# Optimization experiments

Hardware: AMD Instinct MI355X
Metric: run time of the kernel (lower is better)

The kernel has to match this reference:

```python
import jax, jax.numpy as jnp
import numpy as np

NUM_EXPERTS = 8
TOP_K = 2
HIDDEN = 1024
INTER = 4096  # ffn_hidden_size; fc1 produces 2*INTER for gated swiglu
TOKENS = 128


def setup_inputs() -> dict:
    key = jax.random.key(0)
    k1, k2, k3, k4 = jax.random.split(key, 4)
    hidden_states = jax.random.normal(k1, (TOKENS, HIDDEN), dtype=jnp.float32)
    routing = jax.random.normal(k2, (TOKENS, NUM_EXPERTS), dtype=jnp.float32)
    # fc1: [E, 2*inter, hidden] (rows 0:inter = up/linear path fed to act, inter:2*inter = gate)
    w1 = jax.random.normal(k3, (NUM_EXPERTS, 2 * INTER, HIDDEN), dtype=jnp.float32) * 0.02
    # fc2: [E, hidden, inter]
    w2 = jax.random.normal(k4, (NUM_EXPERTS, HIDDEN, INTER), dtype=jnp.float32) * 0.02
    return {"hidden_states": hidden_states, "routing": routing, "w1": w1, "w2": w2}


def reference(hidden_states, routing, w1, w2):
    # Top-k routing with renormalization (TRT-LLM RENORMALIZE mode):
    # softmax over all experts, take top-k probs, rescale to sum to 1.
    probs = jax.nn.softmax(routing, axis=-1)                  # [T, E]
    topv, topi = jax.lax.top_k(probs, TOP_K)                  # [T, k]
    scales = topv / jnp.sum(topv, axis=-1, keepdims=True)     # [T, k]

    num_experts = w1.shape[0]
    inter = w2.shape[2]
    out = jnp.zeros_like(hidden_states)
    # Fixed small loop over experts (structurally distinct weights); tokens stay vectorized.
    for e in range(num_experts):
        # combined routing coefficient of expert e for every token (0 if not selected)
        coef = jnp.sum(jnp.where(topi == e, scales, 0.0), axis=-1)   # [T]
        h = jnp.einsum('th,oh->to', hidden_states, w1[e])            # [T, 2*inter]
        act = jax.nn.silu(h[:, :inter]) * h[:, inter:]               # swiglu
        y = jnp.einsum('ti,hi->th', act, w2[e])                      # [T, hidden]
        out = out + coef[:, None] * y
    return out
```

## Files before the change

kernel.cpp:

```cpp
#include <hip/hip_runtime.h>
#include <hip/hip_bf16.h>

#define T_TOK 128
#define N_EXP 8
#define HID   1024
#define INTER 4096

typedef __bf16 bf16x8 __attribute__((ext_vector_type(8)));
typedef __bf16 bf16x4 __attribute__((ext_vector_type(4)));
typedef float  f32x4  __attribute__((ext_vector_type(4)));

__global__ void route_kernel(const float* __restrict__ routing,
                             int* __restrict__ cnt,
                             int* __restrict__ tok,
                             float* __restrict__ scal) {
    int t = threadIdx.x;
    int wave = t >> 6, lane = t & 63;

    float l[N_EXP];
#pragma unroll
    for (int e = 0; e < N_EXP; ++e) l[e] = routing[t * N_EXP + e];

    int i1 = 0; float v1 = l[0];
#pragma unroll
    for (int e = 1; e < N_EXP; ++e) if (l[e] > v1) { v1 = l[e]; i1 = e; }
    int i2 = -1; float v2 = -1e30f;
#pragma unroll
    for (int e = 0; e < N_EXP; ++e) if (e != i1 && l[e] > v2) { v2 = l[e]; i2 = e; }

    float s1 = 1.0f / (1.0f + __expf(v2 - v1));
    float s2 = 1.0f - s1;

    __shared__ unsigned long long wmask[2][N_EXP];
#pragma unroll
    for (int e = 0; e < N_EXP; ++e) {
        bool sel = (i1 == e) || (i2 == e);
        unsigned long long m = __ballot(sel);
        if (lane == 0) wmask[wave][e] = m;
    }
    __syncthreads();
#pragma unroll
    for (int e = 0; e < N_EXP; ++e) {
        bool sel = (i1 == e) || (i2 == e);
        unsigned long long m = __ballot(sel);
        int pre  = __popcll(m & ((1ull << lane) - 1ull));
        int base = (wave == 1) ? __popcll(wmask[0][e]) : 0;
        if (sel) {
            int slot = base + pre;
            tok [e * T_TOK + slot] = t;
            scal[e * T_TOK + slot] = (i1 == e) ? s1 : s2;
        }
        if (t == 0) cnt[e] = __popcll(wmask[0][e]) + __popcll(wmask[1][e]);
    }
}

__global__ void prep_kernel(const float* __restrict__ hidden,
                            const int* __restrict__ cnt,
                            const int* __restrict__ tok,
                            __bf16* __restrict__ abuf) {
    int b = blockIdx.x;
    int e = b >> 7, s = b & 127;
    if (s >= cnt[e]) return;
    int t = tok[e * T_TOK + s];
    const float4* src = (const float4*)(hidden + (size_t)t * HID);
    __bf16* dst = abuf + ((size_t)e * T_TOK + s) * HID;
#pragma unroll
    for (int it = 0; it < 4; ++it) {
        int idx = it * 64 + threadIdx.x;
        float4 v = src[idx];
        bf16x4 pk;
        pk[0] = (__bf16)v.x; pk[1] = (__bf16)v.y;
        pk[2] = (__bf16)v.z; pk[3] = (__bf16)v.w;
        *(bf16x4*)(dst + idx * 4) = pk;
    }
}

__device__ __forceinline__ bf16x8 cvt8(float4 a, float4 b) {
    bf16x8 r;
    r[0] = (__bf16)a.x; r[1] = (__bf16)a.y; r[2] = (__bf16)a.z; r[3] = (__bf16)a.w;
    r[4] = (__bf16)b.x; r[5] = (__bf16)b.y; r[6] = (__bf16)b.z; r[7] = (__bf16)b.w;
    return r;
}

template<int MG>
__device__ __forceinline__ void g1_loop(const float* __restrict__ bl,
                                        const float* __restrict__ bg,
                                        const __bf16* __restrict__ ap,
                                        f32x4* accl, f32x4* accg) {
#pragma unroll 2
    for (int k0 = 0; k0 < HID; k0 += 32) {
        float4 fl0 = *(const float4*)(bl + k0);
        float4 fl1 = *(const float4*)(bl + k0 + 4);
        float4 fg0 = *(const float4*)(bg + k0);
        float4 fg1 = *(const float4*)(bg + k0 + 4);
        bf16x8 A[MG];
#pragma unroll
        for (int m = 0; m < MG; ++m)
            A[m] = *(const bf16x8*)(ap + (size_t)m * 16 * HID + k0);
        bf16x8 BL = cvt8(fl0, fl1);
        bf16x8 BG = cvt8(fg0, fg1);
#pragma unroll
        for (int m = 0; m < MG; ++m) {
            accl[m] = __builtin_amdgcn_mfma_f32_16x16x32_bf16(A[m], BL, accl[m], 0, 0, 0);
            accg[m] = __builtin_amdgcn_mfma_f32_16x16x32_bf16(A[m], BG, accg[m], 0, 0, 0);
        }
    }
}

__global__ __launch_bounds__(256) void gemm1_kernel(
    const float* __restrict__ w1,
    const int* __restrict__ cnt,
    const __bf16* __restrict__ abuf,
    __bf16* __restrict__ act) {
    int bx = blockIdx.x;
    int e  = bx >> 6, nb = bx & 63;
    int wave = threadIdx.x >> 6, lane = threadIdx.x & 63;
    int n0 = nb * 64 + wave * 16;
    int c  = cnt[e];
    if (c == 0) return;
    int mgs = (c + 15) >> 4;
    int lr = lane & 15;
    int lq = lane >> 4;

    const float* bl = w1 + ((size_t)e * 2 * INTER + n0 + lr) * HID + lq * 8;
    const float* bg = bl + (size_t)INTER * HID;
    const __bf16* ap = abuf + ((size_t)e * T_TOK + lr) * HID + lq * 8;

    f32x4 accl[8], accg[8];
#pragma unroll
    for (int m = 0; m < 8; ++m) {
        accl[m] = (f32x4){0.f, 0.f, 0.f, 0.f};
        accg[m] = (f32x4){0.f, 0.f, 0.f, 0.f};
    }

    switch (mgs) {
        case 1: g1_loop<1>(bl, bg, ap, accl, accg); break;
        case 2: g1_loop<2>(bl, bg, ap, accl, accg); break;
        case 3: g1_loop<3>(bl, bg, ap, accl, accg); break;
        case 4: g1_loop<4>(bl, bg, ap, accl, accg); break;
        case 5: g1_loop<5>(bl, bg, ap, accl, accg); break;
        case 6: g1_loop<6>(bl, bg, ap, accl, accg); break;
        case 7: g1_loop<7>(bl, bg, ap, accl, accg); break;
        default: g1_loop<8>(bl, bg, ap, accl, accg); break;
    }

#pragma unroll
    for (int m = 0; m < 8; ++m) {
        if (m * 16 < c) {
#pragma unroll
            for (int r = 0; r < 4; ++r) {
                int slot = m * 16 + lq * 4 + r;
                if (slot < c) {
                    float lin  = accl[m][r];
                    float gate = accg[m][r];
                    float a = lin * (1.0f / (1.0f + __expf(-lin))) * gate;
                    act[((size_t)e * T_TOK + slot) * INTER + n0 + lr] = (__bf16)a;
                }
            }
        }
    }
}

#define KSPLIT 4
#define KCH (INTER / KSPLIT)

template<int MG>
__device__ __forceinline__ void g2_loop(const float* __restrict__ bp,
                                        const __bf16* __restrict__ ap,
                                        f32x4* acc) {
#pragma unroll 2
    for (int k0 = 0; k0 < KCH; k0 += 32) {
        float4 f0 = *(const float4*)(bp + k0);
        float4 f1 = *(const float4*)(bp + k0 + 4);
        bf16x8 A[MG];
#pragma unroll
        for (int m = 0; m < MG; ++m)
            A[m] = *(const bf16x8*)(ap + (size_t)m * 16 * INTER + k0);
        bf16x8 B = cvt8(f0, f1);
#pragma unroll
        for (int m = 0; m < MG; ++m)
            acc[m] = __builtin_amdgcn_mfma_f32_16x16x32_bf16(A[m], B, acc[m], 0, 0, 0);
    }
}

__global__ __launch_bounds__(256) void gemm2_kernel(
    const float* __restrict__ w2,
    const int* __restrict__ cnt,
    const int* __restrict__ tok,
    const float* __restrict__ scal,
    const __bf16* __restrict__ act,
    float* __restrict__ out) {
    int bx = blockIdx.x;
    int ks = bx & (KSPLIT - 1), nb = (bx >> 2) & 15, e = bx >> 6;
    int wave = threadIdx.x >> 6, lane = threadIdx.x & 63;
    int n0 = nb * 64 + wave * 16;
    int c  = cnt[e];
    if (c == 0) return;
    int mgs = (c + 15) >> 4;
    int lr = lane & 15, lq = lane >> 4;

    const float* bp = w2 + ((size_t)e * HID + n0 + lr) * INTER + ks * KCH + lq * 8;
    const __bf16* ap = act + ((size_t)e * T_TOK + lr) * INTER + ks * KCH + lq * 8;

    f32x4 acc[8];
#pragma unroll
    for (int m = 0; m < 8; ++m) acc[m] = (f32x4){0.f, 0.f, 0.f, 0.f};

    switch (mgs) {
        case 1: g2_loop<1>(bp, ap, acc); break;
        case 2: g2_loop<2>(bp, ap, acc); break;
        case 3: g2_loop<3>(bp, ap, acc); break;
        case 4: g2_loop<4>(bp, ap, acc); break;
        case 5: g2_loop<5>(bp, ap, acc); break;
        case 6: g2_loop<6>(bp, ap, acc); break;
        case 7: g2_loop<7>(bp, ap, acc); break;
        default: g2_loop<8>(bp, ap, acc); break;
    }

#pragma unroll
    for (int m = 0; m < 8; ++m) {
        if (m * 16 < c) {
#pragma unroll
            for (int r = 0; r < 4; ++r) {
                int slot = m * 16 + lq * 4 + r;
                if (slot < c) {
                    int   t    = tok [e * T_TOK + slot];
                    float coef = scal[e * T_TOK + slot];
                    atomicAdd(&out[(size_t)t * HID + n0 + lr], coef * acc[m][r]);
                }
            }
        }
    }
}

extern "C" void kernel_launch(void* const* d_in, const int* in_sizes, int n_in,
                              void* d_out, int out_size, void* d_ws, size_t ws_size,
                              hipStream_t stream) {
    const float* hidden  = (const float*)d_in[0];
    const float* routing = (const float*)d_in[1];
    const float* w1      = (const float*)d_in[2];
    const float* w2      = (const float*)d_in[3];
    float* out = (float*)d_out;

    char* ws = (char*)d_ws;
    int*    cnt  = (int*)ws;
    int*    tok  = (int*)(ws + 64);
    float*  scal = (float*)(ws + 64 + 4096);
    __bf16* abuf = (__bf16*)(ws + 16384);
    __bf16* act  = (__bf16*)(ws + 16384 + (size_t)2 * 1024 * 1024);

    hipMemsetAsync(d_out, 0, (size_t)out_size * sizeof(float), stream);

    route_kernel<<<1, 128, 0, stream>>>(routing, cnt, tok, scal);
    prep_kernel<<<N_EXP * T_TOK, 64, 0, stream>>>(hidden, cnt, tok, abuf);
    gemm1_kernel<<<N_EXP * 64, 256, 0, stream>>>(w1, cnt, abuf, act);
    gemm2_kernel<<<N_EXP * 16 * KSPLIT, 256, 0, stream>>>(w2, cnt, tok, scal, act, out);
}
```

Baseline: 484.6 us.

## Stage fp32 weight tiles through swizzled LDS as bf16 with coalesced row loads

Both GEMM kernels stop having each lane load strided 32-byte chunks of fp32 weights straight from global memory. Each block now loads a 64-row by 256-column weight tile with fully coalesced float4 row reads, converts it to bf16, and writes it into XOR-swizzled shared memory. The MFMA fragments are then read from LDS. This is meant to improve global memory coalescing on the weight stream, which dominates traffic. In exchange it adds two barriers per K-chunk with no double buffering, so loads and compute no longer overlap, and it uses more LDS per block.

```diff
diff --git a/kernel.cpp b/kernel.cpp
--- a/kernel.cpp
+++ b/kernel.cpp
@@ -75,35 +75,60 @@
     }
 }
 
-__device__ __forceinline__ bf16x8 cvt8(float4 a, float4 b) {
-    bf16x8 r;
-    r[0] = (__bf16)a.x; r[1] = (__bf16)a.y; r[2] = (__bf16)a.z; r[3] = (__bf16)a.w;
-    r[4] = (__bf16)b.x; r[5] = (__bf16)b.y; r[6] = (__bf16)b.z; r[7] = (__bf16)b.w;
-    return r;
-}
+#define BK1 256
+#define LDS_ROWB (BK1 * 2)
 
 template<int MG>
-__device__ __forceinline__ void g1_loop(const float* __restrict__ bl,
-                                        const float* __restrict__ bg,
+__device__ __forceinline__ void g1_body(const float* __restrict__ pl,
+                                        const float* __restrict__ pg,
                                         const __bf16* __restrict__ ap,
-                                        f32x4* accl, f32x4* accg) {
-#pragma unroll 2
-    for (int k0 = 0; k0 < HID; k0 += 32) {
-        float4 fl0 = *(const float4*)(bl + k0);
-        float4 fl1 = *(const float4*)(bl + k0 + 4);
-        float4 fg0 = *(const float4*)(bg + k0);
-        float4 fg1 = *(const float4*)(bg + k0 + 4);
-        bf16x8 A[MG];
-#pragma unroll
-        for (int m = 0; m < MG; ++m)
-            A[m] = *(const bf16x8*)(ap + (size_t)m * 16 * HID + k0);
-        bf16x8 BL = cvt8(fl0, fl1);
-        bf16x8 BG = cvt8(fg0, fg1);
-#pragma unroll
-        for (int m = 0; m < MG; ++m) {
-            accl[m] = __builtin_amdgcn_mfma_f32_16x16x32_bf16(A[m], BL, accl[m], 0, 0, 0);
-            accg[m] = __builtin_amdgcn_mfma_f32_16x16x32_bf16(A[m], BG, accg[m], 0, 0, 0);
-        }
+                                        char* __restrict__ ldsb,
+                                        int wave, int lane,
+                                        f32x4* __restrict__ accl,
+                                        f32x4* __restrict__ accg) {
+    const int lr = lane & 15, lq = lane >> 4;
+    const int sread = (lr & 7) << 4;
+    const char* blp = ldsb + (size_t)(wave * 16 + lr) * LDS_ROWB;
+    const char* bgp = blp + (size_t)64 * LDS_ROWB;
+
+    for (int ks = 0; ks < HID; ks += BK1) {
+#pragma unroll 8
+        for (int it = 0; it < 16; ++it) {
+            int row = it * 4 + wave;
+            float4 v = *(const float4*)(pl + (size_t)row * HID + ks);
+            bf16x4 pk;
+            pk[0] = (__bf16)v.x; pk[1] = (__bf16)v.y;
+            pk[2] = (__bf16)v.z; pk[3] = (__bf16)v.w;
+            *(bf16x4*)(ldsb + (size_t)row * LDS_ROWB +
+                       ((lane * 8) ^ ((row & 7) << 4))) = pk;
+        }
+#pragma unroll 8
+        for (int it = 0; it < 16; ++it) {
+            int row = it * 4 + wave;
+            float4 v = *(const float4*)(pg + (size_t)row * HID + ks);
+            bf16x4 pk;
+            pk[0] = (__bf16)v.x; pk[1] = (__bf16)v.y;
+            pk[2] = (__bf16)v.z; pk[3] = (__bf16)v.w;
+            *(bf16x4*)(ldsb + (size_t)(64 + row) * LDS_ROWB +
+                       ((lane * 8) ^ ((row & 7) << 4))) = pk;
+        }
+        __syncthreads();
+#pragma unroll
+        for (int kk = 0; kk < BK1; kk += 32) {
+            int off = (kk * 2 + lq * 16) ^ sread;
+            bf16x8 BL = *(const bf16x8*)(blp + off);
+            bf16x8 BG = *(const bf16x8*)(bgp + off);
+            bf16x8 A[MG];
+#pragma unroll
+            for (int m = 0; m < MG; ++m)
+                A[m] = *(const bf16x8*)(ap + (size_t)m * 16 * HID + ks + kk);
+#pragma unroll
+            for (int m = 0; m < MG; ++m) {
+                accl[m] = __builtin_amdgcn_mfma_f32_16x16x32_bf16(A[m], BL, accl[m], 0, 0, 0);
+                accg[m] = __builtin_amdgcn_mfma_f32_16x16x32_bf16(A[m], BG, accg[m], 0, 0, 0);
+            }
+        }
+        __syncthreads();
     }
 }
 
@@ -112,18 +137,20 @@
     const int* __restrict__ cnt,
     const __bf16* __restrict__ abuf,
     __bf16* __restrict__ act) {
+    __shared__ __align__(16) __bf16 lds[128 * BK1];
     int bx = blockIdx.x;
     int e  = bx >> 6, nb = bx & 63;
     int wave = threadIdx.x >> 6, lane = threadIdx.x & 63;
-    int n0 = nb * 64 + wave * 16;
     int c  = cnt[e];
     if (c == 0) return;
     int mgs = (c + 15) >> 4;
     int lr = lane & 15;
     int lq = lane >> 4;
-
-    const float* bl = w1 + ((size_t)e * 2 * INTER + n0 + lr) * HID + lq * 8;
-    const float* bg = bl + (size_t)INTER * HID;
+    int n0b = nb * 64;
+
+    const float* w1e = w1 + (size_t)e * 2 * INTER * HID;
+    const float* pl  = w1e + (size_t)n0b * HID + lane * 4;
+    const float* pg  = w1e + ((size_t)INTER + n0b) * HID + lane * 4;
     const __bf16* ap = abuf + ((size_t)e * T_TOK + lr) * HID + lq * 8;
 
     f32x4 accl[8], accg[8];
@@ -133,17 +160,19 @@
         accg[m] = (f32x4){0.f, 0.f, 0.f, 0.f};
     }
 
+    char* ldsb = (char*)lds;
     switch (mgs) {
-        case 1: g1_loop<1>(bl, bg, ap, accl, accg); break;
-        case 2: g1_loop<2>(bl, bg, ap, accl, accg); break;
-        case 3: g1_loop<3>(bl, bg, ap, accl, accg); break;
-        case 4: g1_loop<4>(bl, bg, ap, accl, accg); break;
-        case 5: g1_loop<5>(bl, bg, ap, accl, accg); break;
-        case 6: g1_loop<6>(bl, bg, ap, accl, accg); break;
-        case 7: g1_loop<7>(bl, bg, ap, accl, accg); break;
-        default: g1_loop<8>(bl, bg, ap, accl, accg); break;
-    }
-
+        case 1: g1_body<1>(pl, pg, ap, ldsb, wave, lane, accl, accg); break;
+        case 2: g1_body<2>(pl, pg, ap, ldsb, wave, lane, accl, accg); break;
+        case 3: g1_body<3>(pl, pg, ap, ldsb, wave, lane, accl, accg); break;
+        case 4: g1_body<4>(pl, pg, ap, ldsb, wave, lane, accl, accg); break;
+        case 5: g1_body<5>(pl, pg, ap, ldsb, wave, lane, accl, accg); break;
+        case 6: g1_body<6>(pl, pg, ap, ldsb, wave, lane, accl, accg); break;
+        case 7: g1_body<7>(pl, pg, ap, ldsb, wave, lane, accl, accg); break;
+        default: g1_body<8>(pl, pg, ap, ldsb, wave, lane, accl, accg); break;
+    }
+
+    int n0 = n0b + wave * 16;
 #pragma unroll
     for (int m = 0; m < 8; ++m) {
         if (m * 16 < c) {
@@ -165,21 +194,40 @@
 #define KCH (INTER / KSPLIT)
 
 template<int MG>
-__device__ __forceinline__ void g2_loop(const float* __restrict__ bp,
+__device__ __forceinline__ void g2_body(const float* __restrict__ pw,
                                         const __bf16* __restrict__ ap,
-                                        f32x4* acc) {
-#pragma unroll 2
-    for (int k0 = 0; k0 < KCH; k0 += 32) {
-        float4 f0 = *(const float4*)(bp + k0);
-        float4 f1 = *(const float4*)(bp + k0 + 4);
-        bf16x8 A[MG];
-#pragma unroll
-        for (int m = 0; m < MG; ++m)
-            A[m] = *(const bf16x8*)(ap + (size_t)m * 16 * INTER + k0);
-        bf16x8 B = cvt8(f0, f1);
-#pragma unroll
-        for (int m = 0; m < MG; ++m)
-            acc[m] = __builtin_amdgcn_mfma_f32_16x16x32_bf16(A[m], B, acc[m], 0, 0, 0);
+                                        char* __restrict__ ldsb,
+                                        int wave, int lane,
+                                        f32x4* __restrict__ acc) {
+    const int lr = lane & 15, lq = lane >> 4;
+    const int sread = (lr & 7) << 4;
+    const char* bp = ldsb + (size_t)(wave * 16 + lr) * LDS_ROWB;
+
+    for (int ks = 0; ks < KCH; ks += BK1) {
+#pragma unroll 8
+        for (int it = 0; it < 16; ++it) {
+            int row = it * 4 + wave;
+            float4 v = *(const float4*)(pw + (size_t)row * INTER + ks);
+            bf16x4 pk;
+            pk[0] = (__bf16)v.x; pk[1] = (__bf16)v.y;
+            pk[2] = (__bf16)v.z; pk[3] = (__bf16)v.w;
+            *(bf16x4*)(ldsb + (size_t)row * LDS_ROWB +
+                       ((lane * 8) ^ ((row & 7) << 4))) = pk;
+        }
+        __syncthreads();
+#pragma unroll
+        for (int kk = 0; kk < BK1; kk += 32) {
+            int off = (kk * 2 + lq * 16) ^ sread;
+            bf16x8 B = *(const bf16x8*)(bp + off);
+            bf16x8 A[MG];
+#pragma unroll
+            for (int m = 0; m < MG; ++m)
+                A[m] = *(const bf16x8*)(ap + (size_t)m * 16 * INTER + ks + kk);
+#pragma unroll
+            for (int m = 0; m < MG; ++m)
+                acc[m] = __builtin_amdgcn_mfma_f32_16x16x32_bf16(A[m], B, acc[m], 0, 0, 0);
+        }
+        __syncthreads();
     }
 }
 
@@ -190,33 +238,36 @@
     const float* __restrict__ scal,
     const __bf16* __restrict__ act,
     float* __restrict__ out) {
+    __shared__ __align__(16) __bf16 lds[64 * BK1];
     int bx = blockIdx.x;
-    int ks = bx & (KSPLIT - 1), nb = (bx >> 2) & 15, e = bx >> 6;
+    int ksc = bx & (KSPLIT - 1), nb = (bx >> 2) & 15, e = bx >> 6;
     int wave = threadIdx.x >> 6, lane = threadIdx.x & 63;
-    int n0 = nb * 64 + wave * 16;
     int c  = cnt[e];
     if (c == 0) return;
     int mgs = (c + 15) >> 4;
     int lr = lane & 15, lq = lane >> 4;
-
-    const float* bp = w2 + ((size_t)e * HID + n0 + lr) * INTER + ks * KCH + lq * 8;
-    const __bf16* ap = act + ((size_t)e * T_TOK + lr) * INTER + ks * KCH + lq * 8;
+    int n0b = nb * 64;
+
+    const float* pw  = w2 + ((size_t)e * HID + n0b) * INTER + ksc * KCH + lane * 4;
+    const __bf16* ap = act + ((size_t)e * T_TOK + lr) * INTER + ksc * KCH + lq * 8;
 
     f32x4 acc[8];
 #pragma unroll
     for (int m = 0; m < 8; ++m) acc[m] = (f32x4){0.f, 0.f, 0.f, 0.f};
 
+    char* ldsb = (char*)lds;
     switch (mgs) {
-        case 1: g2_loop<1>(bp, ap, acc); break;
-        case 2: g2_loop<2>(bp, ap, acc); break;
-        case 3: g2_loop<3>(bp, ap, acc); break;
-        case 4: g2_loop<4>(bp, ap, acc); break;
-        case 5: g2_loop<5>(bp, ap, acc); break;
-        case 6: g2_loop<6>(bp, ap, acc); break;
-        case 7: g2_loop<7>(bp, ap, acc); break;
-        default: g2_loop<8>(bp, ap, acc); break;
-    }
-
+        case 1: g2_body<1>(pw, ap, ldsb, wave, lane, acc); break;
+        case 2: g2_body<2>(pw, ap, ldsb, wave, lane, acc); break;
+        case 3: g2_body<3>(pw, ap, ldsb, wave, lane, acc); break;
+        case 4: g2_body<4>(pw, ap, ldsb, wave, lane, acc); break;
+        case 5: g2_body<5>(pw, ap, ldsb, wave, lane, acc); break;
+        case 6: g2_body<6>(pw, ap, ldsb, wave, lane, acc); break;
+        case 7: g2_body<7>(pw, ap, ldsb, wave, lane, acc); break;
+        default: g2_body<8>(pw, ap, ldsb, wave, lane, acc); break;
+    }
+
+    int n0 = n0b + wave * 16;
 #pragma unroll
     for (int m = 0; m < 8; ++m) {
         if (m * 16 < c) {
```

Result: no change. 483.7 us (-0.2%).

## Stage fp32 weights through double-buffered LDS via async global_load_lds

Applied to the files above, without the earlier changes.

Both GEMM kernels now stream fp32 weight tiles into a double-buffered LDS ring using the direct global-to-LDS load builtin, with an XOR swizzle on the 16-byte chunk index to avoid bank conflicts. Each wave then reads its B fragments from LDS and converts them to bf16 for the MFMA instructions. The goal is to overlap weight fetches with compute and issue wider, more coalesced reads for the memory-bound weight stream. In exchange it adds per-stage block barriers and 64KB or 32KB of LDS per block, which may lower occupancy.

```diff
diff --git a/kernel.cpp b/kernel.cpp
--- a/kernel.cpp
+++ b/kernel.cpp
@@ -9,6 +9,11 @@
 typedef __bf16 bf16x8 __attribute__((ext_vector_type(8)));
 typedef __bf16 bf16x4 __attribute__((ext_vector_type(4)));
 typedef float  f32x4  __attribute__((ext_vector_type(4)));
+
+#define GLOAD_LDS16(gp, lp)                                                   \
+    __builtin_amdgcn_global_load_lds(                                         \
+        (const __attribute__((address_space(1))) void*)(gp),                  \
+        (__attribute__((address_space(3))) void*)(lp), 16, 0, 0)
 
 __global__ void route_kernel(const float* __restrict__ routing,
                              int* __restrict__ cnt,
@@ -82,28 +87,60 @@
     return r;
 }
 
+
+__device__ __forceinline__ void g1_stage(const char* pe, const char* po,
+                                         char* dstbase, int ksb) {
+#pragma unroll
+    for (int i = 0; i < 8; ++i) {
+        const char* src = ((i & 1) ? po : pe) + (size_t)(i * 4) * (HID * 4) + ksb;
+        GLOAD_LDS16(src, dstbase + i * 1024);
+    }
+}
+
 template<int MG>
-__device__ __forceinline__ void g1_loop(const float* __restrict__ bl,
-                                        const float* __restrict__ bg,
-                                        const __bf16* __restrict__ ap,
-                                        f32x4* accl, f32x4* accg) {
-#pragma unroll 2
-    for (int k0 = 0; k0 < HID; k0 += 32) {
-        float4 fl0 = *(const float4*)(bl + k0);
-        float4 fl1 = *(const float4*)(bl + k0 + 4);
-        float4 fg0 = *(const float4*)(bg + k0);
-        float4 fg1 = *(const float4*)(bg + k0 + 4);
+__device__ __forceinline__ void g1_compute(const char* __restrict__ buf,
+                                           const __bf16* __restrict__ ap,
+                                           int ksf, int wave, int lr,
+                                           const int* __restrict__ coff,
+                                           f32x4* __restrict__ accl,
+                                           f32x4* __restrict__ accg) {
+    const char* rowL = buf + (size_t)(wave * 16 + lr) * 256;
+    const char* rowG = rowL + 64 * 256;
+#pragma unroll
+    for (int kk = 0; kk < 2; ++kk) {
+        float4 l0 = *(const float4*)(rowL + coff[kk * 2]);
+        float4 l1 = *(const float4*)(rowL + coff[kk * 2 + 1]);
+        float4 g0 = *(const float4*)(rowG + coff[kk * 2]);
+        float4 g1 = *(const float4*)(rowG + coff[kk * 2 + 1]);
+        bf16x8 BL = cvt8(l0, l1);
+        bf16x8 BG = cvt8(g0, g1);
         bf16x8 A[MG];
 #pragma unroll
         for (int m = 0; m < MG; ++m)
-            A[m] = *(const bf16x8*)(ap + (size_t)m * 16 * HID + k0);
-        bf16x8 BL = cvt8(fl0, fl1);
-        bf16x8 BG = cvt8(fg0, fg1);
+            A[m] = *(const bf16x8*)(ap + (size_t)m * 16 * HID + ksf + kk * 32);
 #pragma unroll
         for (int m = 0; m < MG; ++m) {
             accl[m] = __builtin_amdgcn_mfma_f32_16x16x32_bf16(A[m], BL, accl[m], 0, 0, 0);
             accg[m] = __builtin_amdgcn_mfma_f32_16x16x32_bf16(A[m], BG, accg[m], 0, 0, 0);
         }
+    }
+}
+
+template<int MG>
+__device__ __forceinline__ void g1_pipe(const char* pe, const char* po,
+                                        char* ldsbase, int ldrow_off,
+                                        const __bf16* ap, const int* coff,
+                                        int wave, int lr,
+                                        f32x4* accl, f32x4* accg) {
+    g1_stage(pe, po, ldsbase + ldrow_off, 0);
+    __syncthreads();
+#pragma unroll 2
+    for (int s = 0; s < 16; ++s) {
+        int b = s & 1;
+        if (s + 1 < 16)
+            g1_stage(pe, po, ldsbase + (b ^ 1) * 32768 + ldrow_off, (s + 1) * 256);
+        g1_compute<MG>(ldsbase + b * 32768, ap, s * 64, wave, lr, coff, accl, accg);
+        __syncthreads();
     }
 }
 
@@ -112,18 +149,33 @@
     const int* __restrict__ cnt,
     const __bf16* __restrict__ abuf,
     __bf16* __restrict__ act) {
+    __shared__ __align__(16) char lds[2 * 32768];
     int bx = blockIdx.x;
     int e  = bx >> 6, nb = bx & 63;
     int wave = threadIdx.x >> 6, lane = threadIdx.x & 63;
-    int n0 = nb * 64 + wave * 16;
     int c  = cnt[e];
     if (c == 0) return;
     int mgs = (c + 15) >> 4;
     int lr = lane & 15;
     int lq = lane >> 4;
-
-    const float* bl = w1 + ((size_t)e * 2 * INTER + n0 + lr) * HID + lq * 8;
-    const float* bg = bl + (size_t)INTER * HID;
+    int n0b = nb * 64;
+
+    int lhi = lane >> 4;
+    int lch = lane & 15;
+    int half = wave & 1, gate = wave >> 1;
+    const char* w1b  = (const char*)w1 + (size_t)e * 2 * INTER * HID * 4;
+    const char* srcb = w1b + ((size_t)gate * INTER + n0b + half * 32 + lhi) * (size_t)(HID * 4);
+    const char* pe = srcb + ((lch ^ lhi) << 4);
+    const char* po = srcb + ((lch ^ (4 + lhi)) << 4);
+    int ldrow_off = (half * 32 + gate * 64) * 256;
+
+    int coff[4];
+#pragma unroll
+    for (int kk = 0; kk < 2; ++kk)
+#pragma unroll
+        for (int j = 0; j < 2; ++j)
+            coff[kk * 2 + j] = ((kk * 8 + lq * 2 + j) ^ (lr & 7)) << 4;
+
     const __bf16* ap = abuf + ((size_t)e * T_TOK + lr) * HID + lq * 8;
 
     f32x4 accl[8], accg[8];
@@ -134,16 +186,17 @@
     }
 
     switch (mgs) {
-        case 1: g1_loop<1>(bl, bg, ap, accl, accg); break;
-        case 2: g1_loop<2>(bl, bg, ap, accl, accg); break;
-        case 3: g1_loop<3>(bl, bg, ap, accl, accg); break;
-        case 4: g1_loop<4>(bl, bg, ap, accl, accg); break;
-        case 5: g1_loop<5>(bl, bg, ap, accl, accg); break;
-        case 6: g1_loop<6>(bl, bg, ap, accl, accg); break;
-        case 7: g1_loop<7>(bl, bg, ap, accl, accg); break;
-        default: g1_loop<8>(bl, bg, ap, accl, accg); break;
-    }
-
+        case 1: g1_pipe<1>(pe, po, lds, ldrow_off, ap, coff, wave, lr, accl, accg); break;
+        case 2: g1_pipe<2>(pe, po, lds, ldrow_off, ap, coff, wave, lr, accl, accg); break;
+        case 3: g1_pipe<3>(pe, po, lds, ldrow_off, ap, coff, wave, lr, accl, accg); break;
+        case 4: g1_pipe<4>(pe, po, lds, ldrow_off, ap, coff, wave, lr, accl, accg); break;
+        case 5: g1_pipe<5>(pe, po, lds, ldrow_off, ap, coff, wave, lr, accl, accg); break;
+        case 6: g1_pipe<6>(pe, po, lds, ldrow_off, ap, coff, wave, lr, accl, accg); break;
+        case 7: g1_pipe<7>(pe, po, lds, ldrow_off, ap, coff, wave, lr, accl, accg); break;
+        default: g1_pipe<8>(pe, po, lds, ldrow_off, ap, coff, wave, lr, accl, accg); break;
+    }
+
+    int n0 = n0b + wave * 16;
 #pragma unroll
     for (int m = 0; m < 8; ++m) {
         if (m * 16 < c) {
@@ -152,8 +205,8 @@
                 int slot = m * 16 + lq * 4 + r;
                 if (slot < c) {
                     float lin  = accl[m][r];
-                    float gate = accg[m][r];
-                    float a = lin * (1.0f / (1.0f + __expf(-lin))) * gate;
+                    float gate_v = accg[m][r];
+                    float a = lin * (1.0f / (1.0f + __expf(-lin))) * gate_v;
                     act[((size_t)e * T_TOK + slot) * INTER + n0 + lr] = (__bf16)a;
                 }
             }
@@ -164,22 +217,52 @@
 #define KSPLIT 4
 #define KCH (INTER / KSPLIT)
 
+__device__ __forceinline__ void g2_stage(const char* pe, const char* po,
+                                         char* dstbase, int ksb) {
+#pragma unroll
+    for (int i = 0; i < 4; ++i) {
+        const char* src = ((i & 1) ? po : pe) + (size_t)(i * 4) * (INTER * 4) + ksb;
+        GLOAD_LDS16(src, dstbase + i * 1024);
+    }
+}
+
 template<int MG>
-__device__ __forceinline__ void g2_loop(const float* __restrict__ bp,
-                                        const __bf16* __restrict__ ap,
-                                        f32x4* acc) {
-#pragma unroll 2
-    for (int k0 = 0; k0 < KCH; k0 += 32) {
-        float4 f0 = *(const float4*)(bp + k0);
-        float4 f1 = *(const float4*)(bp + k0 + 4);
+__device__ __forceinline__ void g2_compute(const char* __restrict__ buf,
+                                           const __bf16* __restrict__ ap,
+                                           int ksf, int wave, int lr,
+                                           const int* __restrict__ coff,
+                                           f32x4* __restrict__ acc) {
+    const char* row = buf + (size_t)(wave * 16 + lr) * 256;
+#pragma unroll
+    for (int kk = 0; kk < 2; ++kk) {
+        float4 q0 = *(const float4*)(row + coff[kk * 2]);
+        float4 q1 = *(const float4*)(row + coff[kk * 2 + 1]);
+        bf16x8 B = cvt8(q0, q1);
         bf16x8 A[MG];
 #pragma unroll
         for (int m = 0; m < MG; ++m)
-            A[m] = *(const bf16x8*)(ap + (size_t)m * 16 * INTER + k0);
-        bf16x8 B = cvt8(f0, f1);
+            A[m] = *(const bf16x8*)(ap + (size_t)m * 16 * INTER + ksf + kk * 32);
 #pragma unroll
         for (int m = 0; m < MG; ++m)
             acc[m] = __builtin_amdgcn_mfma_f32_16x16x32_bf16(A[m], B, acc[m], 0, 0, 0);
+    }
+}
+
+template<int MG>
+__device__ __forceinline__ void g2_pipe(const char* pe, const char* po,
+                                        char* ldsbase, int ldrow_off,
+                                        const __bf16* ap, const int* coff,
+                                        int wave, int lr,
+                                        f32x4* acc) {
+    g2_stage(pe, po, ldsbase + ldrow_off, 0);
+    __syncthreads();
+#pragma unroll 2
+    for (int s = 0; s < 16; ++s) {
+        int b = s & 1;
+        if (s + 1 < 16)
+            g2_stage(pe, po, ldsbase + (b ^ 1) * 16384 + ldrow_off, (s + 1) * 256);
+        g2_compute<MG>(ldsbase + b * 16384, ap, s * 64, wave, lr, coff, acc);
+        __syncthreads();
     }
 }
 
@@ -190,33 +273,50 @@
     const float* __restrict__ scal,
     const __bf16* __restrict__ act,
     float* __restrict__ out) {
+    __shared__ __align__(16) char lds[2 * 16384];
     int bx = blockIdx.x;
-    int ks = bx & (KSPLIT - 1), nb = (bx >> 2) & 15, e = bx >> 6;
+    int ksc = bx & (KSPLIT - 1), nb = (bx >> 2) & 15, e = bx >> 6;
     int wave = threadIdx.x >> 6, lane = threadIdx.x & 63;
-    int n0 = nb * 64 + wave * 16;
     int c  = cnt[e];
     if (c == 0) return;
     int mgs = (c + 15) >> 4;
     int lr = lane & 15, lq = lane >> 4;
-
-    const float* bp = w2 + ((size_t)e * HID + n0 + lr) * INTER + ks * KCH + lq * 8;
-    const __bf16* ap = act + ((size_t)e * T_TOK + lr) * INTER + ks * KCH + lq * 8;
+    int n0b = nb * 64;
+
+    int lhi = lane >> 4;
+    int lch = lane & 15;
+    const char* srcb = (const char*)w2 +
+        ((size_t)e * HID + n0b + wave * 16 + lhi) * (size_t)(INTER * 4) +
+        (size_t)ksc * (KCH * 4);
+    const char* pe = srcb + ((lch ^ lhi) << 4);
+    const char* po = srcb + ((lch ^ (4 + lhi)) << 4);
+    int ldrow_off = wave * 4096;
+
+    int coff[4];
+#pragma unroll
+    for (int kk = 0; kk < 2; ++kk)
+#pragma unroll
+        for (int j = 0; j < 2; ++j)
+            coff[kk * 2 + j] = ((kk * 8 + lq * 2 + j) ^ (lr & 7)) << 4;
+
+    const __bf16* ap = act + ((size_t)e * T_TOK + lr) * INTER + ksc * KCH + lq * 8;
 
     f32x4 acc[8];
 #pragma unroll
     for (int m = 0; m < 8; ++m) acc[m] = (f32x4){0.f, 0.f, 0.f, 0.f};
 
     switch (mgs) {
-        case 1: g2_loop<1>(bp, ap, acc); break;
-        case 2: g2_loop<2>(bp, ap, acc); break;
-        case 3: g2_loop<3>(bp, ap, acc); break;
-        case 4: g2_loop<4>(bp, ap, acc); break;
-        case 5: g2_loop<5>(bp, ap, acc); break;
-        case 6: g2_loop<6>(bp, ap, acc); break;
-        case 7: g2_loop<7>(bp, ap, acc); break;
-        default: g2_loop<8>(bp, ap, acc); break;
-    }
-
+        case 1: g2_pipe<1>(pe, po, lds, ldrow_off, ap, coff, wave, lr, acc); break;
+        case 2: g2_pipe<2>(pe, po, lds, ldrow_off, ap, coff, wave, lr, acc); break;
+        case 3: g2_pipe<3>(pe, po, lds, ldrow_off, ap, coff, wave, lr, acc); break;
+        case 4: g2_pipe<4>(pe, po, lds, ldrow_off, ap, coff, wave, lr, acc); break;
+        case 5: g2_pipe<5>(pe, po, lds, ldrow_off, ap, coff, wave, lr, acc); break;
+        case 6: g2_pipe<6>(pe, po, lds, ldrow_off, ap, coff, wave, lr, acc); break;
+        case 7: g2_pipe<7>(pe, po, lds, ldrow_off, ap, coff, wave, lr, acc); break;
+        default: g2_pipe<8>(pe, po, lds, ldrow_off, ap, coff, wave, lr, acc); break;
+    }
+
+    int n0 = n0b + wave * 16;
 #pragma unroll
     for (int m = 0; m < 8; ++m) {
         if (m * 16 < c) {
```

After: 483.1 us. About the same (-0.3%).
